# Optimization experiments

Hardware: AMD Instinct MI355X
Metric: run time of the kernel (lower is better)

Reference implementation:

```python
import jax, jax.numpy as jnp
import numpy as np

EPS = 1e-05
KEEP_RATIO = 0.7


def setup_inputs() -> dict:
    key = jax.random.key(0)
    ks = jax.random.split(key, 10)
    B, C, L, H = 8, 512, 8192, 128
    return {
        "x": jax.random.normal(ks[0], (B, C, L), dtype=jnp.float32),
        "c": jax.random.normal(ks[1], (B, C, L), dtype=jnp.float32),
        "gw1": jax.random.normal(ks[2], (H, C), dtype=jnp.float32) * 0.05,
        "gb1": jax.random.normal(ks[3], (H,), dtype=jnp.float32) * 0.05,
        "gw2": jax.random.normal(ks[4], (C, H), dtype=jnp.float32) * 0.05,
        "gb2": jax.random.normal(ks[5], (C,), dtype=jnp.float32) * 0.05,
        "mw1": jax.random.normal(ks[6], (H, C), dtype=jnp.float32) * 0.05,
        "mb1": jax.random.normal(ks[7], (H,), dtype=jnp.float32) * 0.05,
        "mw2": jax.random.normal(ks[8], (2 * C, H), dtype=jnp.float32) * 0.05,
        "mb2": jax.random.normal(ks[9], (2 * C,), dtype=jnp.float32) * 0.05,
    }


def reference(x, c, gw1, gb1, gw2, gb2, mw1, mb1, mw2, mb2):
    B, C, L = x.shape
    # per-channel stats over L
    mu_c = jnp.mean(x, axis=2, keepdims=True)                 # [B,C,1]
    var_c = jnp.var(x, axis=2, keepdims=True)                 # ddof=0
    sigma_c = jnp.sqrt(var_c + EPS)
    # per-sample stats over (C,L)
    mu_l = jnp.mean(x, axis=(1, 2), keepdims=True)            # [B,1,1]
    var_l = jnp.var(x, axis=(1, 2), keepdims=True)
    sigma_l = jnp.sqrt(var_l + EPS)
    # gate network on c (1x1 convs == channel matmuls), then mean over L
    h = jax.nn.relu(jnp.einsum('hc,bcl->bhl', gw1, c) + gb1[None, :, None])
    g = jax.nn.sigmoid(jnp.einsum('ch,bhl->bcl', gw2, h) + gb2[None, :, None])
    g_mix = jnp.mean(g, axis=2, keepdims=True)                # [B,C,1]
    mu = g_mix * mu_c + (1.0 - g_mix) * mu_l
    sigma = g_mix * sigma_c + (1.0 - g_mix) * sigma_l
    x_hat = (x - mu) / sigma
    # MLP on pooled condition -> gamma, beta
    cond_pool = jnp.mean(c, axis=2)                           # [B,C]
    hm = jax.nn.relu(jnp.einsum('hc,bc->bh', mw1, cond_pool) + mb1)
    gamma_beta = jnp.einsum('oh,bh->bo', mw2, hm) + mb2       # [B,2C]
    gamma = gamma_beta[:, :C][:, :, None]                     # [B,C,1]
    beta = gamma_beta[:, C:][:, :, None]
    y = (1.0 + gamma) * x_hat + beta
    # top-k channel mask by mean |y| over L
    imp = jnp.mean(jnp.abs(y), axis=2)                        # [B,C]
    k = max(1, int(C * KEEP_RATIO))
    _, idx = jax.lax.top_k(imp, k)                            # [B,k]
    mask = jnp.zeros((B, C), dtype=y.dtype).at[jnp.arange(B)[:, None], idx].set(1.0)
    return y * mask[:, :, None]
```

## Files before the change

### kernel.cpp

```cpp
#include <hip/hip_runtime.h>
#include <hip/hip_bf16.h>
#include <math.h>

#define NB 8
#define NC 512
#define NL 8192
#define NH 128
#define FEPS 1e-5f
#define NKEEP 358

typedef __attribute__((ext_vector_type(8))) short short8;
typedef __attribute__((ext_vector_type(4))) float f32x4;

__device__ __forceinline__ unsigned short f2bf(float x) {
  unsigned u = __float_as_uint(x);
  return (unsigned short)((u + 0x7fffu + ((u >> 16) & 1u)) >> 16);
}
__device__ __forceinline__ unsigned pack2(float a, float b) {
  return (unsigned)f2bf(a) | ((unsigned)f2bf(b) << 16);
}

__global__ __launch_bounds__(256) void k1_xstats(
    const float* __restrict__ x, float* __restrict__ xsum, float* __restrict__ xsumsq,
    const float* __restrict__ gw1, const float* __restrict__ gw2,
    unsigned short* __restrict__ gw1b, unsigned short* __restrict__ gw2b,
    float* __restrict__ csum, float* __restrict__ gsum) {
  const int bc = blockIdx.x;
  const int t = threadIdx.x;
  if (bc < 256) {
    const int i = bc * 256 + t;
    gw1b[i] = f2bf(gw1[i]);
    gw2b[i] = f2bf(gw2[i]);
    if (i < NB * NC) { csum[i] = 0.f; gsum[i] = 0.f; }
  }
  const float4* xp = reinterpret_cast<const float4*>(x + (size_t)bc * NL);
  float s1 = 0.f, s2 = 0.f;
#pragma unroll
  for (int i = 0; i < 8; ++i) {
    float4 v = xp[i * 256 + t];
    s1 += v.x + v.y + v.z + v.w;
    s2 += v.x * v.x + v.y * v.y + v.z * v.z + v.w * v.w;
  }
  for (int off = 32; off; off >>= 1) { s1 += __shfl_down(s1, off); s2 += __shfl_down(s2, off); }
  __shared__ float r1[4], r2[4];
  if ((t & 63) == 0) { r1[t >> 6] = s1; r2[t >> 6] = s2; }
  __syncthreads();
  if (t == 0) {
    xsum[bc]   = r1[0] + r1[1] + r1[2] + r1[3];
    xsumsq[bc] = r2[0] + r2[1] + r2[2] + r2[3];
  }
}

__global__ __launch_bounds__(256, 2) void k2_gate(
    const float* __restrict__ cin,
    const unsigned short* __restrict__ gw1b, const unsigned short* __restrict__ gw2b,
    const float* __restrict__ gb1, const float* __restrict__ gb2,
    float* __restrict__ gsum_g, float* __restrict__ csum_g) {
  __shared__ __align__(16) unsigned AsU[2 * 128 * 36];
  __shared__ __align__(16) unsigned short Hts[4][32][136];
  __shared__ float gsum_s[NC], csum_s[NC], gb2_s[NC];
  __shared__ float gb1_s[NH];

  const int t = threadIdx.x;
  const int lane = t & 63;
  const int w = t >> 6;
  const int r = lane & 15;
  const int kg = lane >> 4;
  const int b = blockIdx.x >> 6;
  const int l0 = (blockIdx.x & 63) * 128;

  const int p = t >> 3;
  const int q = t & 7;

  f32x4 acc0[8], acc1[8];
#pragma unroll
  for (int i = 0; i < 8; ++i) { acc0[i] = (f32x4){0.f,0.f,0.f,0.f}; acc1[i] = (f32x4){0.f,0.f,0.f,0.f}; }

  const float* cbase = cin + (size_t)b * NC * NL + l0;
  const unsigned short* gw1r = gw1b + (size_t)r * NC + kg * 8;

  f32x4 va[4], vb[4];

#define LOADA(kch) { \
    _Pragma("unroll") \
    for (int pass = 0; pass < 4; ++pass) { \
      const float* cp0 = cbase + (size_t)((kch) * 64 + 2 * p) * NL + 32 * pass + 4 * q; \
      va[pass] = __builtin_nontemporal_load(reinterpret_cast<const f32x4*>(cp0)); \
      vb[pass] = __builtin_nontemporal_load(reinterpret_cast<const f32x4*>(cp0 + NL)); \
    } }

#define WRITEA(kch, bufi) { \
    unsigned* dst = AsU + (bufi) * (128 * 36); \
    float sa = 0.f, sb = 0.f; \
    _Pragma("unroll") \
    for (int pass = 0; pass < 4; ++pass) { \
      const int ll = 32 * pass + 4 * q; \
      sa += va[pass].x + va[pass].y + va[pass].z + va[pass].w; \
      sb += vb[pass].x + vb[pass].y + vb[pass].z + vb[pass].w; \
      dst[(ll + 0) * 36 + p] = pack2(va[pass].x, vb[pass].x); \
      dst[(ll + 1) * 36 + p] = pack2(va[pass].y, vb[pass].y); \
      dst[(ll + 2) * 36 + p] = pack2(va[pass].z, vb[pass].z); \
      dst[(ll + 3) * 36 + p] = pack2(va[pass].w, vb[pass].w); \
    } \
    sa += __shfl_xor(sa, 1); sa += __shfl_xor(sa, 2); sa += __shfl_xor(sa, 4); \
    sb += __shfl_xor(sb, 1); sb += __shfl_xor(sb, 2); sb += __shfl_xor(sb, 4); \
    if ((lane & 7) == 0) { \
      atomicAdd(&csum_s[(kch) * 64 + 2 * p],     sa); \
      atomicAdd(&csum_s[(kch) * 64 + 2 * p + 1], sb); \
    } }

  LOADA(0)
  for (int i = t; i < NC; i += 256) { gsum_s[i] = 0.f; csum_s[i] = 0.f; gb2_s[i] = gb2[i]; }
  if (t < NH) gb1_s[t] = gb1[t];
  __syncthreads();
  WRITEA(0, 0)
  __syncthreads();

  for (int k = 0; k < 8; ++k) {
    const int cur = k & 1;
    if (k < 7) LOADA(k + 1)
    const unsigned* Abuf = AsU + cur * (128 * 36);
#pragma unroll
    for (int kk = 0; kk < 2; ++kk) {
      const short8 a0 = *reinterpret_cast<const short8*>(&Abuf[(32 * w + r)      * 36 + 16 * kk + 4 * kg]);
      const short8 a1 = *reinterpret_cast<const short8*>(&Abuf[(32 * w + 16 + r) * 36 + 16 * kk + 4 * kg]);
#pragma unroll
      for (int ht = 0; ht < 8; ++ht) {
        const short8 bf = *reinterpret_cast<const short8*>(
            gw1r + (size_t)(ht * 16) * NC + k * 64 + kk * 32);
        acc0[ht] = __builtin_amdgcn_mfma_f32_16x16x32_bf16(a0, bf, acc0[ht], 0, 0, 0);
        acc1[ht] = __builtin_amdgcn_mfma_f32_16x16x32_bf16(a1, bf, acc1[ht], 0, 0, 0);
      }
    }
    if (k < 7) WRITEA(k + 1, cur ^ 1)
    __syncthreads();
  }

#pragma unroll
  for (int ht = 0; ht < 8; ++ht) {
    const float bias = gb1_s[16 * ht + r];
#pragma unroll
    for (int reg = 0; reg < 4; ++reg) {
      Hts[w][4 * kg + reg][16 * ht + r]      = f2bf(fmaxf(acc0[ht][reg] + bias, 0.f));
      Hts[w][16 + 4 * kg + reg][16 * ht + r] = f2bf(fmaxf(acc1[ht][reg] + bias, 0.f));
    }
  }
  short8 af0[4], af1[4];
#pragma unroll
  for (int kk = 0; kk < 4; ++kk) {
    af0[kk] = *reinterpret_cast<const short8*>(&Hts[w][r][32 * kk + 8 * kg]);
    af1[kk] = *reinterpret_cast<const short8*>(&Hts[w][16 + r][32 * kk + 8 * kg]);
  }

  unsigned short* Bs2 = reinterpret_cast<unsigned short*>(AsU);
  const int crow = lane >> 4;
  const int bs2  = lane & 15;
  short8 bv[4];

#define LOADB2(ccn) { \
    _Pragma("unroll") \
    for (int j = 0; j < 4; ++j) { \
      const int cl = 16 * w + 4 * j + crow; \
      bv[j] = *reinterpret_cast<const short8*>(gw2b + (size_t)((ccn) * 64 + cl) * NH + bs2 * 8); \
    } }
#define WRITEB2(ccn) { \
    unsigned short* dstb = Bs2 + ((ccn) & 1) * 8192; \
    _Pragma("unroll") \
    for (int j = 0; j < 4; ++j) { \
      const int cl = 16 * w + 4 * j + crow; \
      *reinterpret_cast<short8*>(&dstb[cl * 128 + ((bs2 ^ (cl & 7)) * 8)]) = bv[j]; \
    } }

  LOADB2(0)
  WRITEB2(0)
  __syncthreads();
  for (int cc = 0; cc < 8; ++cc) {
    if (cc < 7) LOADB2(cc + 1)
    const unsigned short* Bbuf = Bs2 + (cc & 1) * 8192;
#pragma unroll
    for (int ctt = 0; ctt < 4; ++ctt) {
      f32x4 z0 = (f32x4){0.f,0.f,0.f,0.f}, z1 = (f32x4){0.f,0.f,0.f,0.f};
#pragma unroll
      for (int kk = 0; kk < 4; ++kk) {
        const short8 bf = *reinterpret_cast<const short8*>(
            &Bbuf[(16 * ctt + r) * 128 + (((4 * kk + kg) ^ (r & 7)) * 8)]);
        z0 = __builtin_amdgcn_mfma_f32_16x16x32_bf16(af0[kk], bf, z0, 0, 0, 0);
        z1 = __builtin_amdgcn_mfma_f32_16x16x32_bf16(af1[kk], bf, z1, 0, 0, 0);
      }
      const float bias = gb2_s[cc * 64 + 16 * ctt + r];
      float s = 0.f;
#pragma unroll
      for (int reg = 0; reg < 4; ++reg) {
        s += 1.f / (1.f + __expf(-(z0[reg] + bias)));
        s += 1.f / (1.f + __expf(-(z1[reg] + bias)));
      }
      s += __shfl_xor(s, 16);
      s += __shfl_xor(s, 32);
      if (lane < 16) atomicAdd(&gsum_s[cc * 64 + 16 * ctt + lane], s);
    }
    if (cc < 7) WRITEB2(cc + 1)
    __syncthreads();
  }
  for (int i = t; i < NC; i += 256) {
    atomicAdd(&gsum_g[b * NC + i], gsum_s[i]);
    atomicAdd(&csum_g[b * NC + i], csum_s[i]);
  }
}

__global__ __launch_bounds__(256) void k3_final(
    const float* __restrict__ xsum, const float* __restrict__ xsumsq,
    const float* __restrict__ csum, const float* __restrict__ gsum,
    const float* __restrict__ mw1, const float* __restrict__ mb1,
    const float* __restrict__ mw2, const float* __restrict__ mb2,
    float* __restrict__ a_arr, float* __restrict__ d_arr) {
  __shared__ __align__(16) float cp[NC];
  __shared__ __align__(16) float hm[NH];
  __shared__ float gbv[2 * NC];
  __shared__ double red[8];
  __shared__ float mu_l_s, sig_l_s;
  const int b = blockIdx.x, t = threadIdx.x;

  double s1 = 0.0, s2 = 0.0;
  for (int c = t; c < NC; c += 256) { s1 += (double)xsum[b * NC + c]; s2 += (double)xsumsq[b * NC + c]; }
  for (int off = 32; off; off >>= 1) { s1 += __shfl_down(s1, off); s2 += __shfl_down(s2, off); }
  if ((t & 63) == 0) { red[(t >> 6) * 2] = s1; red[(t >> 6) * 2 + 1] = s2; }
  for (int c = t; c < NC; c += 256) cp[c] = csum[b * NC + c] * (1.f / NL);
  __syncthreads();
  if (t == 0) {
    double S1 = red[0] + red[2] + red[4] + red[6];
    double S2 = red[1] + red[3] + red[5] + red[7];
    double n = (double)NC * NL;
    double mu = S1 / n;
    double var = S2 / n - mu * mu;
    mu_l_s = (float)mu;
    sig_l_s = (float)sqrt(var + (double)FEPS);
  }
  __syncthreads();
  if (t < NH) {
    const float4* row = reinterpret_cast<const float4*>(mw1 + (size_t)t * NC);
    const float4* cpv = reinterpret_cast<const float4*>(cp);
    float acc = mb1[t];
    for (int i = 0; i < NC / 4; ++i) {
      float4 wv = row[i], xv = cpv[i];
      acc += wv.x * xv.x + wv.y * xv.y + wv.z * xv.z + wv.w * xv.w;
    }
    hm[t] = fmaxf(acc, 0.f);
  }
  __syncthreads();
  for (int o = t; o < 2 * NC; o += 256) {
    const float4* row = reinterpret_cast<const float4*>(mw2 + (size_t)o * NH);
    const float4* hv = reinterpret_cast<const float4*>(hm);
    float acc = mb2[o];
    for (int i = 0; i < NH / 4; ++i) {
      float4 wv = row[i], xv = hv[i];
      acc += wv.x * xv.x + wv.y * xv.y + wv.z * xv.z + wv.w * xv.w;
    }
    gbv[o] = acc;
  }
  __syncthreads();
  const float mu_l = mu_l_s, sig_l = sig_l_s;
  for (int c = t; c < NC; c += 256) {
    float gm = gsum[b * NC + c] * (1.f / NL);
    double mu_c = (double)xsum[b * NC + c] / NL;
    double var_c = (double)xsumsq[b * NC + c] / NL - mu_c * mu_c;
    float sig_c = (float)sqrt(var_c + (double)FEPS);
    float mu = gm * (float)mu_c + (1.f - gm) * mu_l;
    float sg = gm * sig_c + (1.f - gm) * sig_l;
    float gamma = gbv[c], beta = gbv[NC + c];
    float A = (1.f + gamma) / sg;
    a_arr[b * NC + c] = A;
    d_arr[b * NC + c] = beta - A * mu;
  }
}

__global__ __launch_bounds__(256) void k4_y(
    const float* __restrict__ x, const float* __restrict__ a_arr,
    const float* __restrict__ d_arr, float* __restrict__ out, float* __restrict__ imp) {
  const int bc = blockIdx.x, t = threadIdx.x;
  const float A = a_arr[bc], D = d_arr[bc];
  const f32x4* xp = reinterpret_cast<const f32x4*>(x + (size_t)bc * NL);
  f32x4* op = reinterpret_cast<f32x4*>(out + (size_t)bc * NL);
  float s = 0.f;
#pragma unroll
  for (int i = 0; i < 8; ++i) {
    f32x4 v = __builtin_nontemporal_load(xp + i * 256 + t);
    f32x4 y;
    y.x = fmaf(A, v.x, D); y.y = fmaf(A, v.y, D);
    y.z = fmaf(A, v.z, D); y.w = fmaf(A, v.w, D);
    s += fabsf(y.x) + fabsf(y.y) + fabsf(y.z) + fabsf(y.w);
    __builtin_nontemporal_store(y, op + i * 256 + t);
  }
  for (int off = 32; off; off >>= 1) s += __shfl_down(s, off);
  __shared__ float rs[4];
  if ((t & 63) == 0) rs[t >> 6] = s;
  __syncthreads();
  if (t == 0) imp[bc] = rs[0] + rs[1] + rs[2] + rs[3];
}

__global__ __launch_bounds__(256) void k5_apply(
    const float* __restrict__ imp, float* __restrict__ out) {
  const int bc = blockIdx.x;
  const int b = bc >> 9;
  const int c = bc & (NC - 1);
  const int t = threadIdx.x;
  const float* row = imp + b * NC;
  const float mine = row[c];
  int cnt = 0;
#pragma unroll
  for (int jj = 0; jj < 2; ++jj) {
    const int j = jj * 256 + t;
    const float o = row[j];
    cnt += (o > mine) || (o == mine && j < c);
  }
  for (int off = 32; off; off >>= 1) cnt += __shfl_down(cnt, off);
  __shared__ int rs[4];
  if ((t & 63) == 0) rs[t >> 6] = cnt;
  __syncthreads();
  const int rank = rs[0] + rs[1] + rs[2] + rs[3];
  if (rank < NKEEP) return;
  f32x4* op = reinterpret_cast<f32x4*>(out + (size_t)bc * NL);
  const f32x4 z = (f32x4){0.f, 0.f, 0.f, 0.f};
#pragma unroll
  for (int i = 0; i < 8; ++i) __builtin_nontemporal_store(z, op + i * 256 + t);
}

extern "C" void kernel_launch(void* const* d_in, const int* in_sizes, int n_in,
                              void* d_out, int out_size, void* d_ws, size_t ws_size,
                              hipStream_t stream) {
  const float* x   = (const float*)d_in[0];
  const float* c   = (const float*)d_in[1];
  const float* gw1 = (const float*)d_in[2];
  const float* gb1 = (const float*)d_in[3];
  const float* gw2 = (const float*)d_in[4];
  const float* gb2 = (const float*)d_in[5];
  const float* mw1 = (const float*)d_in[6];
  const float* mb1 = (const float*)d_in[7];
  const float* mw2 = (const float*)d_in[8];
  const float* mb2 = (const float*)d_in[9];
  float* out = (float*)d_out;
  char* ws = (char*)d_ws;

  unsigned short* gw1b = (unsigned short*)(ws);
  unsigned short* gw2b = (unsigned short*)(ws + 131072);
  float* xsum   = (float*)(ws + 262144);
  float* xsumsq = (float*)(ws + 278528);
  float* csum   = (float*)(ws + 294912);
  float* gsum   = (float*)(ws + 311296);
  float* a_arr  = (float*)(ws + 327680);
  float* d_arr  = (float*)(ws + 344064);
  float* imp    = (float*)(ws + 360448);

  k1_xstats<<<NB * NC, 256, 0, stream>>>(x, xsum, xsumsq, gw1, gw2, gw1b, gw2b, csum, gsum);
  k2_gate<<<NB * (NL / 128), 256, 0, stream>>>(c, gw1b, gw2b, gb1, gb2, gsum, csum);
  k3_final<<<NB, 256, 0, stream>>>(xsum, xsumsq, csum, gsum, mw1, mb1, mw2, mb2, a_arr, d_arr);
  k4_y<<<NB * NC, 256, 0, stream>>>(x, a_arr, d_arr, out, imp);
  k5_apply<<<NB * NC, 256, 0, stream>>>(imp, out);
}
```

Baseline: 175.9 us.

## Prefetch condition tiles two chunks ahead and hoist weight loads before MFMAs

The gate GEMM loop now keeps two register buffers of `c` tiles, so global loads are issued two K-chunks ahead instead of one. The LDS write for the next chunk is moved before the MFMA block. All gw1 B-fragments for the chunk are loaded up front. The `__syncthreads` is replaced by an LDS-only waitcnt plus `s_barrier`, with sched barriers around it, so outstanding global loads are not drained at each barrier. The aim is to hide HBM latency behind MFMA work, at the cost of extra VGPRs for the second buffer and the fragment arrays, which may lower occupancy or cause spills.

```diff
diff --git a/kernel.cpp b/kernel.cpp
--- a/kernel.cpp
+++ b/kernel.cpp
@@ -79,28 +79,28 @@
   const float* cbase = cin + (size_t)b * NC * NL + l0;
   const unsigned short* gw1r = gw1b + (size_t)r * NC + kg * 8;
 
-  f32x4 va[4], vb[4];
-
-#define LOADA(kch) { \
+  f32x4 vaA[4], vbA[4], vaB[4], vbB[4];
+
+#define LOADA(dA, dB, kch) { \
     _Pragma("unroll") \
     for (int pass = 0; pass < 4; ++pass) { \
       const float* cp0 = cbase + (size_t)((kch) * 64 + 2 * p) * NL + 32 * pass + 4 * q; \
-      va[pass] = __builtin_nontemporal_load(reinterpret_cast<const f32x4*>(cp0)); \
-      vb[pass] = __builtin_nontemporal_load(reinterpret_cast<const f32x4*>(cp0 + NL)); \
+      dA[pass] = __builtin_nontemporal_load(reinterpret_cast<const f32x4*>(cp0)); \
+      dB[pass] = __builtin_nontemporal_load(reinterpret_cast<const f32x4*>(cp0 + NL)); \
     } }
 
-#define WRITEA(kch, bufi) { \
+#define WRITEA(sA, sB, kch, bufi) { \
     unsigned* dst = AsU + (bufi) * (128 * 36); \
     float sa = 0.f, sb = 0.f; \
     _Pragma("unroll") \
     for (int pass = 0; pass < 4; ++pass) { \
       const int ll = 32 * pass + 4 * q; \
-      sa += va[pass].x + va[pass].y + va[pass].z + va[pass].w; \
-      sb += vb[pass].x + vb[pass].y + vb[pass].z + vb[pass].w; \
-      dst[(ll + 0) * 36 + p] = pack2(va[pass].x, vb[pass].x); \
-      dst[(ll + 1) * 36 + p] = pack2(va[pass].y, vb[pass].y); \
-      dst[(ll + 2) * 36 + p] = pack2(va[pass].z, vb[pass].z); \
-      dst[(ll + 3) * 36 + p] = pack2(va[pass].w, vb[pass].w); \
+      sa += sA[pass].x + sA[pass].y + sA[pass].z + sA[pass].w; \
+      sb += sB[pass].x + sB[pass].y + sB[pass].z + sB[pass].w; \
+      dst[(ll + 0) * 36 + p] = pack2(sA[pass].x, sB[pass].x); \
+      dst[(ll + 1) * 36 + p] = pack2(sA[pass].y, sB[pass].y); \
+      dst[(ll + 2) * 36 + p] = pack2(sA[pass].z, sB[pass].z); \
+      dst[(ll + 3) * 36 + p] = pack2(sA[pass].w, sB[pass].w); \
     } \
     sa += __shfl_xor(sa, 1); sa += __shfl_xor(sa, 2); sa += __shfl_xor(sa, 4); \
     sb += __shfl_xor(sb, 1); sb += __shfl_xor(sb, 2); sb += __shfl_xor(sb, 4); \
@@ -109,31 +109,51 @@
       atomicAdd(&csum_s[(kch) * 64 + 2 * p + 1], sb); \
     } }
 
-  LOADA(0)
+  LOADA(vaA, vbA, 0)
+  LOADA(vaB, vbB, 1)
   for (int i = t; i < NC; i += 256) { gsum_s[i] = 0.f; csum_s[i] = 0.f; gb2_s[i] = gb2[i]; }
   if (t < NH) gb1_s[t] = gb1[t];
   __syncthreads();
-  WRITEA(0, 0)
-  __syncthreads();
+  WRITEA(vaA, vbA, 0, 0)
+  asm volatile("s_waitcnt lgkmcnt(0)" ::: "memory");
+  __builtin_amdgcn_s_barrier();
+  __builtin_amdgcn_sched_barrier(0);
 
   for (int k = 0; k < 8; ++k) {
-    const int cur = k & 1;
-    if (k < 7) LOADA(k + 1)
-    const unsigned* Abuf = AsU + cur * (128 * 36);
+    const unsigned* Abuf = AsU + (k & 1) * (128 * 36);
+    short8 bfr[16];
+#pragma unroll
+    for (int ht = 0; ht < 8; ++ht) {
+      bfr[2 * ht]     = *reinterpret_cast<const short8*>(gw1r + (size_t)(ht * 16) * NC + k * 64);
+      bfr[2 * ht + 1] = *reinterpret_cast<const short8*>(gw1r + (size_t)(ht * 16) * NC + k * 64 + 32);
+    }
+    short8 a0[2], a1[2];
 #pragma unroll
     for (int kk = 0; kk < 2; ++kk) {
-      const short8 a0 = *reinterpret_cast<const short8*>(&Abuf[(32 * w + r)      * 36 + 16 * kk + 4 * kg]);
-      const short8 a1 = *reinterpret_cast<const short8*>(&Abuf[(32 * w + 16 + r) * 36 + 16 * kk + 4 * kg]);
+      a0[kk] = *reinterpret_cast<const short8*>(&Abuf[(32 * w + r)      * 36 + 16 * kk + 4 * kg]);
+      a1[kk] = *reinterpret_cast<const short8*>(&Abuf[(32 * w + 16 + r) * 36 + 16 * kk + 4 * kg]);
+    }
+    __builtin_amdgcn_sched_barrier(0);
+    if (k < 7) {
+      if ((k & 1) == 0) { WRITEA(vaB, vbB, k + 1, 1) } else { WRITEA(vaA, vbA, k + 1, 0) }
+    }
+    __builtin_amdgcn_sched_barrier(0);
+    if (k < 6) {
+      if ((k & 1) == 0) { LOADA(vaA, vbA, k + 2) } else { LOADA(vaB, vbB, k + 2) }
+    }
+    __builtin_amdgcn_sched_barrier(0);
+#pragma unroll
+    for (int kk = 0; kk < 2; ++kk) {
 #pragma unroll
       for (int ht = 0; ht < 8; ++ht) {
-        const short8 bf = *reinterpret_cast<const short8*>(
-            gw1r + (size_t)(ht * 16) * NC + k * 64 + kk * 32);
-        acc0[ht] = __builtin_amdgcn_mfma_f32_16x16x32_bf16(a0, bf, acc0[ht], 0, 0, 0);
-        acc1[ht] = __builtin_amdgcn_mfma_f32_16x16x32_bf16(a1, bf, acc1[ht], 0, 0, 0);
+        acc0[ht] = __builtin_amdgcn_mfma_f32_16x16x32_bf16(a0[kk], bfr[2 * ht + kk], acc0[ht], 0, 0, 0);
+        acc1[ht] = __builtin_amdgcn_mfma_f32_16x16x32_bf16(a1[kk], bfr[2 * ht + kk], acc1[ht], 0, 0, 0);
       }
     }
-    if (k < 7) WRITEA(k + 1, cur ^ 1)
-    __syncthreads();
+    __builtin_amdgcn_sched_barrier(0);
+    asm volatile("s_waitcnt lgkmcnt(0)" ::: "memory");
+    __builtin_amdgcn_s_barrier();
+    __builtin_amdgcn_sched_barrier(0);
   }
 
 #pragma unroll
```

Measured after the change: 170.9 us. 2.8% less time.
